# Performance work log

Measured on AMD Instinct MI355X. Metric: run time of the kernel, lower is better.

Reference implementation:

```python
import jax, jax.numpy as jnp
import numpy as np

N = 100_000      # nodes
E = 1_600_000    # edges (avg degree 16)
DN = 64          # node feature dim
DE = 64          # edge feature dim


def _w(k, shape):
    fan_in = shape[0]
    return jax.random.normal(k, shape, dtype=jnp.float32) / np.sqrt(fan_in)


def setup_inputs() -> dict:
    key = jax.random.key(0)
    ks = jax.random.split(key, 12)
    x = jax.random.normal(ks[0], (N, DN), dtype=jnp.float32)
    e = jax.random.normal(ks[1], (E, DE), dtype=jnp.float32)
    senders = jax.random.randint(ks[2], (E,), 0, N)
    receivers = jax.random.randint(ks[3], (E,), 0, N)
    return {
        "x": x, "e": e, "senders": senders, "receivers": receivers,
        "We1": _w(ks[4], (DE + 2 * DN, DE)), "be1": jnp.zeros((DE,), jnp.float32),
        "We2": _w(ks[5], (DE, DE)),          "be2": jnp.zeros((DE,), jnp.float32),
        "We3": _w(ks[6], (DE, DE)),          "be3": jnp.zeros((DE,), jnp.float32),
        "Wn1": _w(ks[7], (DN + DE, DN)),     "bn1": jnp.zeros((DN,), jnp.float32),
        "Wn2": _w(ks[8], (DN, DN)),          "bn2": jnp.zeros((DN,), jnp.float32),
        "Wn3": _w(ks[9], (DN, DN)),          "bn3": jnp.zeros((DN,), jnp.float32),
    }


def reference(x, e, senders, receivers,
              We1, be1, We2, be2, We3, be3,
              Wn1, bn1, Wn2, bn2, Wn3, bn3):
    # --- EdgeBlock: concat(edge, sender, receiver) -> MLP ---
    h = jnp.concatenate([e, x[senders], x[receivers]], axis=-1)  # [E, DE+2*DN]
    h = jax.nn.relu(h @ We1 + be1)
    h = jax.nn.relu(h @ We2 + be2)
    e_new = h @ We3 + be3                                        # [E, DE]
    # --- NodeBlock: sum-aggregate receiving edges, concat(node, agg) -> MLP ---
    agg = jax.ops.segment_sum(e_new, receivers, num_segments=N)  # [N, DE]
    g = jnp.concatenate([x, agg], axis=-1)                       # [N, DN+DE]
    g = jax.nn.relu(g @ Wn1 + bn1)
    g = jax.nn.relu(g @ Wn2 + bn2)
    x_new = g @ Wn3 + bn3                                        # [N, DN]
    return x_new
```

## Files before the change

kernel.cpp:

```cpp
#include <hip/hip_runtime.h>

#define NN 100000
#define NE 1600000

typedef short v8s __attribute__((ext_vector_type(8)));
typedef float v4f __attribute__((ext_vector_type(4)));
typedef unsigned short v4u16 __attribute__((ext_vector_type(4)));

__device__ __forceinline__ unsigned short f2bf(float f) {
    union { float f; unsigned int u; } v; v.f = f;
    unsigned int r = v.u + 0x7FFFu + ((v.u >> 16) & 1u);
    return (unsigned short)(r >> 16);
}

__device__ __forceinline__ void store_bf4(unsigned short* base, int row, int k, float4 v) {
    v4u16 p;
    p.x = f2bf(v.x); p.y = f2bf(v.y); p.z = f2bf(v.z); p.w = f2bf(v.w);
    *(v4u16*)(base + ((k >> 5) * 2048 + row * 32 + (k & 31))) = p;
}

#define MFMA16(acc, a, b) acc = __builtin_amdgcn_mfma_f32_16x16x32_bf16(a, b, acc, 0, 0, 0)

__global__ __launch_bounds__(256, 2) void edge_kernel(
    const float* __restrict__ x, const float* __restrict__ e,
    const int* __restrict__ snd, const int* __restrict__ rcv,
    const float* __restrict__ We1, const float* __restrict__ be1,
    const float* __restrict__ We2, const float* __restrict__ be2,
    const float* __restrict__ We3, const float* __restrict__ be3,
    float* agg, int numTiles)
{
    extern __shared__ unsigned short smem[];
    unsigned short* WT1 = smem;
    unsigned short* WT2 = WT1 + 12288;
    unsigned short* WT3 = WT2 + 4096;
    unsigned short* A   = WT3 + 4096;

    const int tid = threadIdx.x;

    for (int idx = tid; idx < 192 * 64; idx += 256) {
        int k = idx >> 6, n = idx & 63;
        WT1[(k >> 5) * 2048 + n * 32 + (k & 31)] = f2bf(We1[idx]);
    }
    for (int idx = tid; idx < 64 * 64; idx += 256) {
        int k = idx >> 6, n = idx & 63;
        int off = (k >> 5) * 2048 + n * 32 + (k & 31);
        WT2[off] = f2bf(We2[idx]);
        WT3[off] = f2bf(We3[idx]);
    }

    const int lane = tid & 63;
    const int wv   = tid >> 6;
    const int l15  = lane & 15;
    const int quad = lane >> 4;
    const int astrip = wv * 16;

    float b1v[4], b2v[4], b3v[4];
#pragma unroll
    for (int nt = 0; nt < 4; ++nt) {
        b1v[nt] = be1[nt * 16 + l15];
        b2v[nt] = be2[nt * 16 + l15];
        b3v[nt] = be3[nt * 16 + l15];
    }

    const int arow = (astrip + l15) * 32 + quad * 8;
    const int brow = l15 * 32 + quad * 8;

    __syncthreads();

    for (int tile = blockIdx.x; tile < numTiles; tile += gridDim.x) {
        const int ebase = tile * 64;

#pragma unroll
        for (int t = 0; t < 4; ++t) {
            int idx = tid + t * 256;
            int row = idx >> 4;
            int k0  = (idx & 15) * 4;
            float4 ve = *(const float4*)(e + (size_t)(ebase + row) * 64 + k0);
            store_bf4(A, row, k0, ve);
            int s = snd[ebase + row];
            float4 vs = *(const float4*)(x + (size_t)s * 64 + k0);
            store_bf4(A, row, 64 + k0, vs);
            int r = rcv[ebase + row];
            float4 vr = *(const float4*)(x + (size_t)r * 64 + k0);
            store_bf4(A, row, 128 + k0, vr);
        }
        __syncthreads();

        {
            v4f acc[4];
#pragma unroll
            for (int nt = 0; nt < 4; ++nt) acc[nt] = (v4f){0.f, 0.f, 0.f, 0.f};
#pragma unroll
            for (int kb = 0; kb < 6; ++kb) {
                v8s af = *(const v8s*)(A + kb * 2048 + arow);
#pragma unroll
                for (int nt = 0; nt < 4; ++nt) {
                    v8s bf = *(const v8s*)(WT1 + kb * 2048 + brow + nt * 512);
                    MFMA16(acc[nt], af, bf);
                }
            }
#pragma unroll
            for (int nt = 0; nt < 4; ++nt) {
                int kk = nt * 16 + l15;
#pragma unroll
                for (int r = 0; r < 4; ++r) {
                    int m = astrip + quad * 4 + r;
                    float v = acc[nt][r] + b1v[nt];
                    v = v > 0.f ? v : 0.f;
                    A[(kk >> 5) * 2048 + m * 32 + (kk & 31)] = f2bf(v);
                }
            }
        }

        {
            v4f acc[4];
#pragma unroll
            for (int nt = 0; nt < 4; ++nt) acc[nt] = (v4f){0.f, 0.f, 0.f, 0.f};
#pragma unroll
            for (int kb = 0; kb < 2; ++kb) {
                v8s af = *(const v8s*)(A + kb * 2048 + arow);
#pragma unroll
                for (int nt = 0; nt < 4; ++nt) {
                    v8s bf = *(const v8s*)(WT2 + kb * 2048 + brow + nt * 512);
                    MFMA16(acc[nt], af, bf);
                }
            }
#pragma unroll
            for (int nt = 0; nt < 4; ++nt) {
                int kk = nt * 16 + l15;
#pragma unroll
                for (int r = 0; r < 4; ++r) {
                    int m = astrip + quad * 4 + r;
                    float v = acc[nt][r] + b2v[nt];
                    v = v > 0.f ? v : 0.f;
                    A[(2 + (kk >> 5)) * 2048 + m * 32 + (kk & 31)] = f2bf(v);
                }
            }
        }

        {
            v4f acc[4];
#pragma unroll
            for (int nt = 0; nt < 4; ++nt) acc[nt] = (v4f){0.f, 0.f, 0.f, 0.f};
#pragma unroll
            for (int kb = 0; kb < 2; ++kb) {
                v8s af = *(const v8s*)(A + (2 + kb) * 2048 + arow);
#pragma unroll
                for (int nt = 0; nt < 4; ++nt) {
                    v8s bf = *(const v8s*)(WT3 + kb * 2048 + brow + nt * 512);
                    MFMA16(acc[nt], af, bf);
                }
            }
#pragma unroll
            for (int r = 0; r < 4; ++r) {
                int el = astrip + quad * 4 + r;
                int dst = rcv[ebase + el];
                float* aggrow = agg + (size_t)dst * 64;
#pragma unroll
                for (int nt = 0; nt < 4; ++nt) {
                    unsafeAtomicAdd(aggrow + nt * 16 + l15, acc[nt][r] + b3v[nt]);
                }
            }
        }
        __syncthreads();
    }
}

__global__ __launch_bounds__(256, 2) void node_kernel(
    const float* __restrict__ x,
    const float* __restrict__ Wn1, const float* __restrict__ bn1,
    const float* __restrict__ Wn2, const float* __restrict__ bn2,
    const float* __restrict__ Wn3, const float* __restrict__ bn3,
    float* aggout)
{
    extern __shared__ unsigned short smem[];
    unsigned short* WT1 = smem;
    unsigned short* WT2 = WT1 + 8192;
    unsigned short* WT3 = WT2 + 4096;
    unsigned short* A   = WT3 + 4096;

    const int tid = threadIdx.x;

    for (int idx = tid; idx < 128 * 64; idx += 256) {
        int k = idx >> 6, n = idx & 63;
        WT1[(k >> 5) * 2048 + n * 32 + (k & 31)] = f2bf(Wn1[idx]);
    }
    for (int idx = tid; idx < 64 * 64; idx += 256) {
        int k = idx >> 6, n = idx & 63;
        int off = (k >> 5) * 2048 + n * 32 + (k & 31);
        WT2[off] = f2bf(Wn2[idx]);
        WT3[off] = f2bf(Wn3[idx]);
    }

    const int lane = tid & 63;
    const int wv   = tid >> 6;
    const int l15  = lane & 15;
    const int quad = lane >> 4;
    const int astrip = wv * 16;

    float b1v[4], b2v[4], b3v[4];
#pragma unroll
    for (int nt = 0; nt < 4; ++nt) {
        b1v[nt] = bn1[nt * 16 + l15];
        b2v[nt] = bn2[nt * 16 + l15];
        b3v[nt] = bn3[nt * 16 + l15];
    }

    const int arow = (astrip + l15) * 32 + quad * 8;
    const int brow = l15 * 32 + quad * 8;
    const int nbase = blockIdx.x * 64;

    __syncthreads();

#pragma unroll
    for (int t = 0; t < 4; ++t) {
        int idx = tid + t * 256;
        int row = idx >> 4;
        int k0  = (idx & 15) * 4;
        int node = nbase + row;
        float4 vx = {0.f, 0.f, 0.f, 0.f}, va = {0.f, 0.f, 0.f, 0.f};
        if (node < NN) {
            vx = *(const float4*)(x + (size_t)node * 64 + k0);
            va = *(const float4*)(aggout + (size_t)node * 64 + k0);
        }
        store_bf4(A, row, k0, vx);
        store_bf4(A, row, 64 + k0, va);
    }
    __syncthreads();

    {
        v4f acc[4];
#pragma unroll
        for (int nt = 0; nt < 4; ++nt) acc[nt] = (v4f){0.f, 0.f, 0.f, 0.f};
#pragma unroll
        for (int kb = 0; kb < 4; ++kb) {
            v8s af = *(const v8s*)(A + kb * 2048 + arow);
#pragma unroll
            for (int nt = 0; nt < 4; ++nt) {
                v8s bf = *(const v8s*)(WT1 + kb * 2048 + brow + nt * 512);
                MFMA16(acc[nt], af, bf);
            }
        }
#pragma unroll
        for (int nt = 0; nt < 4; ++nt) {
            int kk = nt * 16 + l15;
#pragma unroll
            for (int r = 0; r < 4; ++r) {
                int m = astrip + quad * 4 + r;
                float v = acc[nt][r] + b1v[nt];
                v = v > 0.f ? v : 0.f;
                A[(kk >> 5) * 2048 + m * 32 + (kk & 31)] = f2bf(v);
            }
        }
    }

    {
        v4f acc[4];
#pragma unroll
        for (int nt = 0; nt < 4; ++nt) acc[nt] = (v4f){0.f, 0.f, 0.f, 0.f};
#pragma unroll
        for (int kb = 0; kb < 2; ++kb) {
            v8s af = *(const v8s*)(A + kb * 2048 + arow);
#pragma unroll
            for (int nt = 0; nt < 4; ++nt) {
                v8s bf = *(const v8s*)(WT2 + kb * 2048 + brow + nt * 512);
                MFMA16(acc[nt], af, bf);
            }
        }
#pragma unroll
        for (int nt = 0; nt < 4; ++nt) {
            int kk = nt * 16 + l15;
#pragma unroll
            for (int r = 0; r < 4; ++r) {
                int m = astrip + quad * 4 + r;
                float v = acc[nt][r] + b2v[nt];
                v = v > 0.f ? v : 0.f;
                A[(2 + (kk >> 5)) * 2048 + m * 32 + (kk & 31)] = f2bf(v);
            }
        }
    }

    {
        v4f acc[4];
#pragma unroll
        for (int nt = 0; nt < 4; ++nt) acc[nt] = (v4f){0.f, 0.f, 0.f, 0.f};
#pragma unroll
        for (int kb = 0; kb < 2; ++kb) {
            v8s af = *(const v8s*)(A + (2 + kb) * 2048 + arow);
#pragma unroll
            for (int nt = 0; nt < 4; ++nt) {
                v8s bf = *(const v8s*)(WT3 + kb * 2048 + brow + nt * 512);
                MFMA16(acc[nt], af, bf);
            }
        }
#pragma unroll
        for (int r = 0; r < 4; ++r) {
            int node = nbase + astrip + quad * 4 + r;
            if (node < NN) {
#pragma unroll
                for (int nt = 0; nt < 4; ++nt) {
                    aggout[(size_t)node * 64 + nt * 16 + l15] = acc[nt][r] + b3v[nt];
                }
            }
        }
    }
}

extern "C" void kernel_launch(void* const* d_in, const int* in_sizes, int n_in,
                              void* d_out, int out_size, void* d_ws, size_t ws_size,
                              hipStream_t stream) {
    const float* x   = (const float*)d_in[0];
    const float* e   = (const float*)d_in[1];
    const int*   snd = (const int*)d_in[2];
    const int*   rcv = (const int*)d_in[3];
    const float* We1 = (const float*)d_in[4];  const float* be1 = (const float*)d_in[5];
    const float* We2 = (const float*)d_in[6];  const float* be2 = (const float*)d_in[7];
    const float* We3 = (const float*)d_in[8];  const float* be3 = (const float*)d_in[9];
    const float* Wn1 = (const float*)d_in[10]; const float* bn1 = (const float*)d_in[11];
    const float* Wn2 = (const float*)d_in[12]; const float* bn2 = (const float*)d_in[13];
    const float* Wn3 = (const float*)d_in[14]; const float* bn3 = (const float*)d_in[15];
    float* out = (float*)d_out;

    hipMemsetAsync(out, 0, (size_t)NN * 64 * sizeof(float), stream);

    edge_kernel<<<512, 256, 65536, stream>>>(x, e, snd, rcv,
                                             We1, be1, We2, be2, We3, be3,
                                             out, NE / 64);

    node_kernel<<<(NN + 63) / 64, 256, 49152, stream>>>(x,
                                                        Wn1, bn1, Wn2, bn2, Wn3, bn3,
                                                        out);
}
```

Baseline: 873.0 us.

## Process edges per wave with register-fed MFMA operands and swizzled LDS

Measured after the change: 854.7 us. 1.02x faster.

```diff
diff --git a/kernel.cpp b/kernel.cpp
--- a/kernel.cpp
+++ b/kernel.cpp
@@ -2,6 +2,7 @@
 
 #define NN 100000
 #define NE 1600000
+#define NT (NE / 16)
 
 typedef short v8s __attribute__((ext_vector_type(8)));
 typedef float v4f __attribute__((ext_vector_type(4)));
@@ -13,6 +14,20 @@
     return (unsigned short)(r >> 16);
 }
 
+__device__ __forceinline__ v8s pack8(float4 a, float4 b) {
+    union { v8s v; unsigned short u[8]; } t;
+    t.u[0] = f2bf(a.x); t.u[1] = f2bf(a.y); t.u[2] = f2bf(a.z); t.u[3] = f2bf(a.w);
+    t.u[4] = f2bf(b.x); t.u[5] = f2bf(b.y); t.u[6] = f2bf(b.z); t.u[7] = f2bf(b.w);
+    return t.v;
+}
+
+__device__ __forceinline__ int wfrag(int row, int k) {
+    return row * 32 + ((((k >> 3) & 3) ^ ((row >> 1) & 3)) << 3) + (k & 7);
+}
+__device__ __forceinline__ int hoff(int m, int k) {
+    return (k >> 5) * 512 + m * 32 + ((((k >> 3) & 3) ^ ((m >> 1) & 3)) << 3) + (k & 7);
+}
+
 __device__ __forceinline__ void store_bf4(unsigned short* base, int row, int k, float4 v) {
     v4u16 p;
     p.x = f2bf(v.x); p.y = f2bf(v.y); p.z = f2bf(v.z); p.w = f2bf(v.w);
@@ -21,29 +36,29 @@
 
 #define MFMA16(acc, a, b) acc = __builtin_amdgcn_mfma_f32_16x16x32_bf16(a, b, acc, 0, 0, 0)
 
-__global__ __launch_bounds__(256, 2) void edge_kernel(
+__global__ __launch_bounds__(512, 4) void edge_kernel(
     const float* __restrict__ x, const float* __restrict__ e,
     const int* __restrict__ snd, const int* __restrict__ rcv,
     const float* __restrict__ We1, const float* __restrict__ be1,
     const float* __restrict__ We2, const float* __restrict__ be2,
     const float* __restrict__ We3, const float* __restrict__ be3,
-    float* agg, int numTiles)
+    float* agg)
 {
     extern __shared__ unsigned short smem[];
     unsigned short* WT1 = smem;
     unsigned short* WT2 = WT1 + 12288;
     unsigned short* WT3 = WT2 + 4096;
-    unsigned short* A   = WT3 + 4096;
+    unsigned short* HS  = WT3 + 4096;
 
     const int tid = threadIdx.x;
 
-    for (int idx = tid; idx < 192 * 64; idx += 256) {
+    for (int idx = tid; idx < 192 * 64; idx += 512) {
         int k = idx >> 6, n = idx & 63;
-        WT1[(k >> 5) * 2048 + n * 32 + (k & 31)] = f2bf(We1[idx]);
-    }
-    for (int idx = tid; idx < 64 * 64; idx += 256) {
+        WT1[(k >> 5) * 2048 + wfrag(n, k & 31)] = f2bf(We1[idx]);
+    }
+    for (int idx = tid; idx < 64 * 64; idx += 512) {
         int k = idx >> 6, n = idx & 63;
-        int off = (k >> 5) * 2048 + n * 32 + (k & 31);
+        int off = (k >> 5) * 2048 + wfrag(n, k & 31);
         WT2[off] = f2bf(We2[idx]);
         WT3[off] = f2bf(We3[idx]);
     }
@@ -52,7 +67,7 @@
     const int wv   = tid >> 6;
     const int l15  = lane & 15;
     const int quad = lane >> 4;
-    const int astrip = wv * 16;
+    unsigned short* H = HS + wv * 1024;
 
     float b1v[4], b2v[4], b3v[4];
 #pragma unroll
@@ -62,29 +77,48 @@
         b3v[nt] = be3[nt * 16 + l15];
     }
 
-    const int arow = (astrip + l15) * 32 + quad * 8;
-    const int brow = l15 * 32 + quad * 8;
+    const int swz = l15 * 32 + ((quad ^ ((l15 >> 1) & 3)) << 3);
 
     __syncthreads();
 
-    for (int tile = blockIdx.x; tile < numTiles; tile += gridDim.x) {
-        const int ebase = tile * 64;
-
-#pragma unroll
-        for (int t = 0; t < 4; ++t) {
-            int idx = tid + t * 256;
-            int row = idx >> 4;
-            int k0  = (idx & 15) * 4;
-            float4 ve = *(const float4*)(e + (size_t)(ebase + row) * 64 + k0);
-            store_bf4(A, row, k0, ve);
-            int s = snd[ebase + row];
-            float4 vs = *(const float4*)(x + (size_t)s * 64 + k0);
-            store_bf4(A, row, 64 + k0, vs);
-            int r = rcv[ebase + row];
-            float4 vr = *(const float4*)(x + (size_t)r * 64 + k0);
-            store_bf4(A, row, 128 + k0, vr);
-        }
-        __syncthreads();
+    const int nwaves = gridDim.x * (blockDim.x >> 6);
+    int wt = blockIdx.x * (blockDim.x >> 6) + wv;
+
+    int er = wt * 16 + l15;
+    int s0 = snd[er], r0 = rcv[er];
+
+    while (wt < NT) {
+        const int ebase = wt * 16;
+        const int s = s0, rcur = r0;
+
+        const float* erow = e + (size_t)(ebase + l15) * 64 + quad * 8;
+        const float* xs   = x + (size_t)s    * 64 + quad * 8;
+        const float* xr   = x + (size_t)rcur * 64 + quad * 8;
+
+        float4 e00 = *(const float4*)(erow);
+        float4 e01 = *(const float4*)(erow + 4);
+        float4 e10 = *(const float4*)(erow + 32);
+        float4 e11 = *(const float4*)(erow + 36);
+        float4 s00 = *(const float4*)(xs);
+        float4 s01 = *(const float4*)(xs + 4);
+        float4 s10 = *(const float4*)(xs + 32);
+        float4 s11 = *(const float4*)(xs + 36);
+        float4 r00 = *(const float4*)(xr);
+        float4 r01 = *(const float4*)(xr + 4);
+        float4 r10 = *(const float4*)(xr + 32);
+        float4 r11 = *(const float4*)(xr + 36);
+
+        const int wtn = wt + nwaves;
+        if (wtn < NT) {
+            int ern = wtn * 16 + l15;
+            s0 = snd[ern];
+            r0 = rcv[ern];
+        }
+
+        v8s af[6];
+        af[0] = pack8(e00, e01); af[1] = pack8(e10, e11);
+        af[2] = pack8(s00, s01); af[3] = pack8(s10, s11);
+        af[4] = pack8(r00, r01); af[5] = pack8(r10, r11);
 
         {
             v4f acc[4];
@@ -92,11 +126,10 @@
             for (int nt = 0; nt < 4; ++nt) acc[nt] = (v4f){0.f, 0.f, 0.f, 0.f};
 #pragma unroll
             for (int kb = 0; kb < 6; ++kb) {
-                v8s af = *(const v8s*)(A + kb * 2048 + arow);
 #pragma unroll
                 for (int nt = 0; nt < 4; ++nt) {
-                    v8s bf = *(const v8s*)(WT1 + kb * 2048 + brow + nt * 512);
-                    MFMA16(acc[nt], af, bf);
+                    v8s bf = *(const v8s*)(WT1 + kb * 2048 + nt * 512 + swz);
+                    MFMA16(acc[nt], af[kb], bf);
                 }
             }
 #pragma unroll
@@ -104,65 +137,63 @@
                 int kk = nt * 16 + l15;
 #pragma unroll
                 for (int r = 0; r < 4; ++r) {
-                    int m = astrip + quad * 4 + r;
                     float v = acc[nt][r] + b1v[nt];
                     v = v > 0.f ? v : 0.f;
-                    A[(kk >> 5) * 2048 + m * 32 + (kk & 31)] = f2bf(v);
+                    H[hoff(quad * 4 + r, kk)] = f2bf(v);
                 }
             }
         }
 
         {
+            v8s a0 = *(const v8s*)(H + swz);
+            v8s a1 = *(const v8s*)(H + 512 + swz);
             v4f acc[4];
 #pragma unroll
             for (int nt = 0; nt < 4; ++nt) acc[nt] = (v4f){0.f, 0.f, 0.f, 0.f};
 #pragma unroll
-            for (int kb = 0; kb < 2; ++kb) {
-                v8s af = *(const v8s*)(A + kb * 2048 + arow);
-#pragma unroll
-                for (int nt = 0; nt < 4; ++nt) {
-                    v8s bf = *(const v8s*)(WT2 + kb * 2048 + brow + nt * 512);
-                    MFMA16(acc[nt], af, bf);
-                }
+            for (int nt = 0; nt < 4; ++nt) {
+                v8s bf0 = *(const v8s*)(WT2 + nt * 512 + swz);
+                MFMA16(acc[nt], a0, bf0);
+                v8s bf1 = *(const v8s*)(WT2 + 2048 + nt * 512 + swz);
+                MFMA16(acc[nt], a1, bf1);
             }
 #pragma unroll
             for (int nt = 0; nt < 4; ++nt) {
                 int kk = nt * 16 + l15;
 #pragma unroll
                 for (int r = 0; r < 4; ++r) {
-                    int m = astrip + quad * 4 + r;
                     float v = acc[nt][r] + b2v[nt];
                     v = v > 0.f ? v : 0.f;
-                    A[(2 + (kk >> 5)) * 2048 + m * 32 + (kk & 31)] = f2bf(v);
+                    H[hoff(quad * 4 + r, kk)] = f2bf(v);
                 }
             }
         }
 
         {
+            v8s a0 = *(const v8s*)(H + swz);
+            v8s a1 = *(const v8s*)(H + 512 + swz);
             v4f acc[4];
 #pragma unroll
             for (int nt = 0; nt < 4; ++nt) acc[nt] = (v4f){0.f, 0.f, 0.f, 0.f};
 #pragma unroll
-            for (int kb = 0; kb < 2; ++kb) {
-                v8s af = *(const v8s*)(A + (2 + kb) * 2048 + arow);
+            for (int nt = 0; nt < 4; ++nt) {
+                v8s bf0 = *(const v8s*)(WT3 + nt * 512 + swz);
+                MFMA16(acc[nt], a0, bf0);
+                v8s bf1 = *(const v8s*)(WT3 + 2048 + nt * 512 + swz);
+                MFMA16(acc[nt], a1, bf1);
+            }
+#pragma unroll
+            for (int ri = 0; ri < 4; ++ri) {
+                int dst = __shfl(rcur, quad * 4 + ri, 16);
+                float* aggrow = agg + (size_t)dst * 64;
 #pragma unroll
                 for (int nt = 0; nt < 4; ++nt) {
-                    v8s bf = *(const v8s*)(WT3 + kb * 2048 + brow + nt * 512);
-                    MFMA16(acc[nt], af, bf);
-                }
-            }
-#pragma unroll
-            for (int r = 0; r < 4; ++r) {
-                int el = astrip + quad * 4 + r;
-                int dst = rcv[ebase + el];
-                float* aggrow = agg + (size_t)dst * 64;
-#pragma unroll
-                for (int nt = 0; nt < 4; ++nt) {
-                    unsafeAtomicAdd(aggrow + nt * 16 + l15, acc[nt][r] + b3v[nt]);
-                }
-            }
-        }
-        __syncthreads();
+                    unsafeAtomicAdd(aggrow + nt * 16 + l15, acc[nt][ri] + b3v[nt]);
+                }
+            }
+        }
+
+        wt = wtn;
     }
 }
 
@@ -323,9 +354,9 @@
 
     hipMemsetAsync(out, 0, (size_t)NN * 64 * sizeof(float), stream);
 
-    edge_kernel<<<512, 256, 65536, stream>>>(x, e, snd, rcv,
+    edge_kernel<<<512, 512, 57344, stream>>>(x, e, snd, rcv,
                                              We1, be1, We2, be2, We3, be3,
-                                             out, NE / 64);
+                                             out);
 
     node_kernel<<<(NN + 63) / 64, 256, 49152, stream>>>(x,
                                                         Wn1, bn1, Wn2, bn2, Wn3, bn3,
```
